# Optimization experiments

Measured on AMD Instinct MI355X. Metric: run time of the kernel, lower is better.

## Reference

```python
import jax, jax.numpy as jnp
import numpy as np

B, S, D = 2, 2048, 1024
H = 16
HD = D // H  # 64

def setup_inputs() -> dict:
    key = jax.random.key(0)
    k1, k2, k3 = jax.random.split(key, 3)
    scale = 0.02
    return {
        "x": jax.random.normal(k1, (B, S, D), dtype=jnp.float32),
        "w_qkv": jax.random.normal(k2, (D, 3 * D), dtype=jnp.float32) * scale,
        "b_qkv": jnp.zeros((3 * D,), dtype=jnp.float32),
        "w_proj": jax.random.normal(k3, (D, D), dtype=jnp.float32) * scale,
        "b_proj": jnp.zeros((D,), dtype=jnp.float32),
    }

def reference(x, w_qkv, b_qkv, w_proj, b_proj):
    batch, seq_len, _ = x.shape
    qkv = x @ w_qkv + b_qkv                      # [B,S,3D]
    qkv = qkv.reshape(batch, seq_len, 3, H, HD)
    qkv = jnp.transpose(qkv, (2, 0, 3, 1, 4))    # [3,B,H,S,HD]
    q, k, v = qkv[0], qkv[1], qkv[2]
    attn = jnp.einsum('bhqd,bhkd->bhqk', q, k) / jnp.sqrt(jnp.float32(HD))
    attn = jax.nn.softmax(attn, axis=-1)         # [B,H,S,S]
    out = jnp.einsum('bhqk,bhkd->bhqd', attn, v)
    out = jnp.transpose(out, (0, 2, 1, 3)).reshape(batch, seq_len, -1)
    return out @ w_proj + b_proj
```

## Files before the change

kernel.cpp:

```cpp
#include <hip/hip_runtime.h>
#include <math.h>

#define SS 2048
#define DD 1024
#define HH 16
#define NQKV 3072
#define MROWS 4096
#define KD 1024

typedef __attribute__((ext_vector_type(8))) short bf16x8;
typedef __attribute__((ext_vector_type(8))) unsigned short us8;
typedef __attribute__((ext_vector_type(4))) float f32x4;
typedef unsigned short u16;
typedef unsigned int u32;

#define SCALE_C 0.18033688011112042f

#define GLDS16(g, l) \
  __builtin_amdgcn_global_load_lds((const __attribute__((address_space(1))) u32*)(g), \
                                   (__attribute__((address_space(3))) u32*)(l), 16, 0, 0)

static __device__ __forceinline__ u16 f2bf(float f) {
  union { float f; u32 u; } v; v.f = f;
  u32 u = v.u;
  u += 0x7fffu + ((u >> 16) & 1u);
  return (u16)(u >> 16);
}
static __device__ __forceinline__ u32 pk2(float a, float b) {
  return (u32)f2bf(a) | ((u32)f2bf(b) << 16);
}
static __device__ __forceinline__ u32 pk2t(float a, float b) {
  union { float f; u32 u; } ua, ub; ua.f = a; ub.f = b;
  return __builtin_amdgcn_perm(ub.u, ua.u, 0x07060302u);
}

__global__ __launch_bounds__(256) void k_prep(const float* __restrict__ x,
                                              const float* __restrict__ w_qkv,
                                              const float* __restrict__ w_proj,
                                              u16* __restrict__ x_bf,
                                              u16* __restrict__ wqkvT,
                                              u16* __restrict__ wprojT) {
  __shared__ float t[64][65];
  int bx = blockIdx.x;
  int tid = threadIdx.x;
  if (bx < 2048) {
    int i = (bx * 256 + tid) * 8;
    float4 a = *(const float4*)(x + i);
    float4 b = *(const float4*)(x + i + 4);
    us8 o;
    o[0] = f2bf(a.x); o[1] = f2bf(a.y); o[2] = f2bf(a.z); o[3] = f2bf(a.w);
    o[4] = f2bf(b.x); o[5] = f2bf(b.y); o[6] = f2bf(b.z); o[7] = f2bf(b.w);
    *(us8*)(x_bf + i) = o;
    return;
  }
  const float* in; u16* out; int R = KD, C, tile;
  if (bx < 2048 + 768) { in = w_qkv; out = wqkvT; C = NQKV; tile = bx - 2048; }
  else                 { in = w_proj; out = wprojT; C = DD; tile = bx - 2816; }
  int tilesC = C >> 6;
  int tc = tile % tilesC, tr = tile / tilesC;
  int r0 = tr * 64, c0 = tc * 64;
  int lx = tid & 63, ly = tid >> 6;
#pragma unroll
  for (int i = 0; i < 16; i++) {
    int rr = ly + i * 4;
    t[rr][lx] = in[(size_t)(r0 + rr) * C + c0 + lx];
  }
  __syncthreads();
#pragma unroll
  for (int i = 0; i < 16; i++) {
    int cc = ly + i * 4;
    out[(size_t)(c0 + cc) * R + r0 + lx] = f2bf(t[lx][cc]);
  }
}

template <int MODE, int BM>
__global__ __launch_bounds__(256, 2) void k_gemm(const u16* __restrict__ A,
                                                 const u16* __restrict__ Bt,
                                                 const float* __restrict__ bias,
                                                 void* __restrict__ Cout,
                                                 u16* __restrict__ vt,
                                                 int M, int N, int K) {
  constexpr int MT = BM / 32;
  __shared__ alignas(16) u16 As[BM * 32];
  __shared__ alignas(16) u16 Bs[128 * 32];
  const int tid = threadIdx.x;
  const int w = tid >> 6, ln = tid & 63;
  const int wm = w >> 1, wn = w & 1;
  const int lm = ln & 15, quad = ln >> 4;
  const int m0 = blockIdx.y * BM, n0 = blockIdx.x * 128;
  const int lr = ln >> 2, c = ln & 3;
  const int cg = c ^ (lr & 3);

  f32x4 acc[MT][4];
#pragma unroll
  for (int i = 0; i < MT; i++)
#pragma unroll
    for (int j = 0; j < 4; j++) acc[i][j] = (f32x4){0.f, 0.f, 0.f, 0.f};

  const u16* gA0 = A  + (size_t)(m0 + 16 * w       + lr) * K + cg * 8;
  const u16* gA1 = A  + (size_t)(m0 + 16 * (w + 4) + lr) * K + cg * 8;
  const u16* gB0 = Bt + (size_t)(n0 + 16 * w       + lr) * K + cg * 8;
  const u16* gB1 = Bt + (size_t)(n0 + 16 * (w + 4) + lr) * K + cg * 8;
  char* lA0 = (char*)As + w * 1024;
  char* lA1 = (char*)As + (w + 4) * 1024;
  char* lB0 = (char*)Bs + w * 1024;
  char* lB1 = (char*)Bs + (w + 4) * 1024;

  for (int k0 = 0; k0 < K; k0 += 32) {
    GLDS16(gA0 + k0, lA0);
    if (BM == 128) GLDS16(gA1 + k0, lA1);
    GLDS16(gB0 + k0, lB0);
    GLDS16(gB1 + k0, lB1);
    __syncthreads();
    bf16x8 af[MT], bfr[4];
#pragma unroll
    for (int t = 0; t < MT; t++)
      af[t]  = *(const bf16x8*)((const char*)As + (wm * (MT * 16) + t * 16 + lm) * 64 + ((quad ^ (lm & 3)) * 16));
#pragma unroll
    for (int t = 0; t < 4; t++)
      bfr[t] = *(const bf16x8*)((const char*)Bs + (wn * 64 + t * 16 + lm) * 64 + ((quad ^ (lm & 3)) * 16));
#pragma unroll
    for (int mt = 0; mt < MT; mt++)
#pragma unroll
      for (int nt = 0; nt < 4; nt++)
        acc[mt][nt] = __builtin_amdgcn_mfma_f32_16x16x32_bf16(af[mt], bfr[nt], acc[mt][nt], 0, 0, 0);
    __syncthreads();
  }

  float bv[4];
#pragma unroll
  for (int nt = 0; nt < 4; nt++) bv[nt] = bias[n0 + wn * 64 + nt * 16 + lm];

  if (MODE == 2 && n0 >= 2 * DD) {
    int b = m0 >> 11;
    int s0 = (m0 & 2047) + wm * 64;
#pragma unroll
    for (int mt = 0; mt < MT; mt++) {
      int s = s0 + mt * 16 + quad * 4;
#pragma unroll
      for (int nt = 0; nt < 4; nt++) {
        int n = n0 + wn * 64 + nt * 16 + lm;
        int bh = b * HH + ((n - 2 * DD) >> 6);
        int d = n & 63;
        uint2 v;
        v.x = pk2(acc[mt][nt][0] + bv[nt], acc[mt][nt][1] + bv[nt]);
        v.y = pk2(acc[mt][nt][2] + bv[nt], acc[mt][nt][3] + bv[nt]);
        *(uint2*)&vt[(size_t)(bh * 64 + d) * SS + s] = v;
      }
    }
    return;
  }

  const float qs = (MODE == 2 && n0 < DD) ? SCALE_C : 1.0f;
#pragma unroll
  for (int mt = 0; mt < MT; mt++) {
#pragma unroll
    for (int r = 0; r < 4; r++) {
      int row = m0 + wm * (MT * 16) + mt * 16 + quad * 4 + r;
#pragma unroll
      for (int nt = 0; nt < 4; nt++) {
        int col = n0 + wn * 64 + nt * 16 + lm;
        float v = (acc[mt][nt][r] + bv[nt]) * qs;
        if (MODE == 2) ((u16*)Cout)[(size_t)row * N + col] = f2bf(v);
        else           ((float*)Cout)[(size_t)row * N + col] = v;
      }
    }
  }
}

__global__ __launch_bounds__(256, 3) void k_attn(const u16* __restrict__ qkv,
                                                 const u16* __restrict__ vt,
                                                 u16* __restrict__ attn) {
  __shared__ alignas(16) u16 Ks[2][64 * 64];
  __shared__ alignas(16) u16 Vs[2][64 * 64];
  __shared__ alignas(16) u16 Ps[4][16][72];

  const int tid = threadIdx.x;
  const int w = tid >> 6, ln = tid & 63;
  const int lm = ln & 15, quad = ln >> 4;
  const int bx = blockIdx.x;
  const int bh = bx >> 5;
  const int q0 = (bx & 31) * 64;
  const int b = bh >> 4, h = bh & 15;
  const size_t qkv_b = (size_t)b * SS * NQKV;
  const int hcol = h * 64;

  const int lr = ln >> 3, cc = ln & 7;
  const int cg = cc ^ lr;

  bf16x8 qf[2];
#pragma unroll
  for (int kk = 0; kk < 2; kk++)
    qf[kk] = *(const bf16x8*)(qkv + qkv_b +
               (size_t)(q0 + w * 16 + lm) * NQKV + hcol + kk * 32 + quad * 8);

  f32x4 o[4];
  float l = 0.f;
#pragma unroll
  for (int t = 0; t < 4; t++) o[t] = (f32x4){0, 0, 0, 0};

  char* psw = (char*)&Ps[w][0][0];

#pragma unroll
  for (int rr = 0; rr < 2; rr++) {
    int i = w + 4 * rr;
    GLDS16(qkv + qkv_b + (size_t)(8 * i + lr) * NQKV + DD + hcol + cg * 8, (char*)Ks[0] + i * 1024);
    GLDS16(vt + (size_t)(bh * 64 + 8 * i + lr) * SS + cg * 8,              (char*)Vs[0] + i * 1024);
  }

#pragma unroll 1
  for (int it = 0; it < SS / 64; it++) {
    __syncthreads();

    if (it + 1 < SS / 64) {
      int kv1 = (it + 1) * 64;
      char* kd = (char*)Ks[(it + 1) & 1];
      char* vd = (char*)Vs[(it + 1) & 1];
#pragma unroll
      for (int rr = 0; rr < 2; rr++) {
        int i = w + 4 * rr;
        GLDS16(qkv + qkv_b + (size_t)(kv1 + 8 * i + lr) * NQKV + DD + hcol + cg * 8, kd + i * 1024);
        GLDS16(vt + (size_t)(bh * 64 + 8 * i + lr) * SS + kv1 + cg * 8,              vd + i * 1024);
      }
    }

    const char* ksb = (const char*)Ks[it & 1];
    const char* vsb = (const char*)Vs[it & 1];

    f32x4 s[4];
#pragma unroll
    for (int t = 0; t < 4; t++) s[t] = (f32x4){0, 0, 0, 0};
#pragma unroll
    for (int kk = 0; kk < 2; kk++)
#pragma unroll
      for (int t = 0; t < 4; t++) {
        bf16x8 kf = *(const bf16x8*)(ksb + (t * 16 + lm) * 128 + (((kk * 4 + quad) ^ (lm & 7)) * 16));
        s[t] = __builtin_amdgcn_mfma_f32_16x16x32_bf16(kf, qf[kk], s[t], 0, 0, 0);
      }

    float sum = 0.f;
    u32 pkv[4][2];
#pragma unroll
    for (int t = 0; t < 4; t++) {
      float p0 = __builtin_amdgcn_exp2f(s[t][0]);
      float p1 = __builtin_amdgcn_exp2f(s[t][1]);
      float p2 = __builtin_amdgcn_exp2f(s[t][2]);
      float p3 = __builtin_amdgcn_exp2f(s[t][3]);
      sum += (p0 + p1) + (p2 + p3);
      pkv[t][0] = pk2t(p0, p1);
      pkv[t][1] = pk2t(p2, p3);
    }
    sum += __shfl_xor(sum, 16);
    sum += __shfl_xor(sum, 32);
    l += sum;
#pragma unroll
    for (int t = 0; t < 4; t++) {
      uint2 v; v.x = pkv[t][0]; v.y = pkv[t][1];
      *(uint2*)(psw + lm * 144 + t * 32 + quad * 8) = v;
    }

#pragma unroll
    for (int kk = 0; kk < 2; kk++) {
      bf16x8 pf = *(const bf16x8*)(psw + lm * 144 + kk * 64 + quad * 16);
#pragma unroll
      for (int t = 0; t < 4; t++) {
        bf16x8 vf = *(const bf16x8*)(vsb + (t * 16 + lm) * 128 + (((kk * 4 + quad) ^ (lm & 7)) * 16));
        o[t] = __builtin_amdgcn_mfma_f32_16x16x32_bf16(vf, pf, o[t], 0, 0, 0);
      }
    }
  }

  float il = 1.0f / l;
  int row = b * SS + q0 + w * 16 + lm;
#pragma unroll
  for (int t = 0; t < 4; t++) {
    uint2 v;
    v.x = pk2(o[t][0] * il, o[t][1] * il);
    v.y = pk2(o[t][2] * il, o[t][3] * il);
    *(uint2*)&attn[(size_t)row * DD + hcol + t * 16 + quad * 4] = v;
  }
}

extern "C" void kernel_launch(void* const* d_in, const int* in_sizes, int n_in,
                              void* d_out, int out_size, void* d_ws, size_t ws_size,
                              hipStream_t stream) {
  const float* x      = (const float*)d_in[0];
  const float* w_qkv  = (const float*)d_in[1];
  const float* b_qkv  = (const float*)d_in[2];
  const float* w_proj = (const float*)d_in[3];
  const float* b_proj = (const float*)d_in[4];
  float* out = (float*)d_out;

  u16* ws     = (u16*)d_ws;
  u16* x_bf   = ws;
  u16* wqkvT  = x_bf   + (size_t)MROWS * KD;
  u16* wprojT = wqkvT  + (size_t)NQKV * KD;
  u16* qkv    = wprojT + (size_t)DD * KD;
  u16* attn   = qkv    + (size_t)MROWS * NQKV;
  u16* vt     = attn   + (size_t)MROWS * DD;

  k_prep<<<3072, 256, 0, stream>>>(x, w_qkv, w_proj, x_bf, wqkvT, wprojT);
  k_gemm<2, 128><<<dim3(NQKV / 128, MROWS / 128), 256, 0, stream>>>(x_bf, wqkvT, b_qkv, qkv, vt, MROWS, NQKV, KD);
  k_attn<<<2 * HH * (SS / 64), 256, 0, stream>>>(qkv, vt, attn);
  k_gemm<0, 64><<<dim3(DD / 128, MROWS / 64), 256, 0, stream>>>(attn, wprojT, b_proj, out, nullptr, MROWS, DD, KD);
}
```

Before: 209.2 us.

## Split attention KV range in two halves with combine kernel, 128-row query tiles

The attention kernel now has each block process 128 query rows (two 16-row sub-tiles per wave) against half of the key/value sequence, so K/V tiles loaded into LDS are reused across twice as many queries. Partial unnormalized outputs and row sums are written to reused workspace buffers (x_bf and wqkvT), and a new combine kernel sums the halves and normalizes. It also swizzles the P scratch layout and raises the occupancy hint. The cost is an extra kernel launch, extra bf16 partial-output traffic, and double rounding of the partials to bf16.

Result: no change. 210.0 us (+0.4%).

```diff
diff --git a/kernel.cpp b/kernel.cpp
--- a/kernel.cpp
+++ b/kernel.cpp
@@ -25,6 +25,9 @@
   u32 u = v.u;
   u += 0x7fffu + ((u >> 16) & 1u);
   return (u16)(u >> 16);
+}
+static __device__ __forceinline__ float bf2f(u16 x) {
+  union { u32 u; float f; } v; v.u = ((u32)x) << 16; return v.f;
 }
 static __device__ __forceinline__ u32 pk2(float a, float b) {
   return (u32)f2bf(a) | ((u32)f2bf(b) << 16);
@@ -168,52 +171,63 @@
   }
 }
 
-__global__ __launch_bounds__(256, 3) void k_attn(const u16* __restrict__ qkv,
+__global__ __launch_bounds__(256, 4) void k_attn(const u16* __restrict__ qkv,
                                                  const u16* __restrict__ vt,
-                                                 u16* __restrict__ attn) {
+                                                 u16* __restrict__ po0,
+                                                 u16* __restrict__ po1,
+                                                 float* __restrict__ lb0,
+                                                 float* __restrict__ lb1) {
   __shared__ alignas(16) u16 Ks[2][64 * 64];
   __shared__ alignas(16) u16 Vs[2][64 * 64];
-  __shared__ alignas(16) u16 Ps[4][16][72];
+  __shared__ alignas(16) u16 Ps[4 * 16 * 64];
 
   const int tid = threadIdx.x;
   const int w = tid >> 6, ln = tid & 63;
   const int lm = ln & 15, quad = ln >> 4;
   const int bx = blockIdx.x;
-  const int bh = bx >> 5;
-  const int q0 = (bx & 31) * 64;
+  const int half = bx >> 9;
+  const int bxx = bx & 511;
+  const int bh = bxx >> 4;
+  const int q0 = (bxx & 15) * 128;
   const int b = bh >> 4, h = bh & 15;
   const size_t qkv_b = (size_t)b * SS * NQKV;
   const int hcol = h * 64;
+  const int kvoff = half * (SS / 2);
+
+  u16* __restrict__ po = half ? po1 : po0;
+  float* __restrict__ lb = half ? lb1 : lb0;
 
   const int lr = ln >> 3, cc = ln & 7;
   const int cg = cc ^ lr;
 
-  bf16x8 qf[2];
-#pragma unroll
-  for (int kk = 0; kk < 2; kk++)
-    qf[kk] = *(const bf16x8*)(qkv + qkv_b +
-               (size_t)(q0 + w * 16 + lm) * NQKV + hcol + kk * 32 + quad * 8);
-
-  f32x4 o[4];
-  float l = 0.f;
-#pragma unroll
-  for (int t = 0; t < 4; t++) o[t] = (f32x4){0, 0, 0, 0};
-
-  char* psw = (char*)&Ps[w][0][0];
+  bf16x8 qf[2][2];
+#pragma unroll
+  for (int qs2 = 0; qs2 < 2; qs2++)
+#pragma unroll
+    for (int kk = 0; kk < 2; kk++)
+      qf[qs2][kk] = *(const bf16x8*)(qkv + qkv_b +
+                     (size_t)(q0 + w * 32 + qs2 * 16 + lm) * NQKV + hcol + kk * 32 + quad * 8);
+
+  f32x4 o[4][2];
+  float l[2] = {0.f, 0.f};
+#pragma unroll
+  for (int t = 0; t < 4; t++) { o[t][0] = (f32x4){0, 0, 0, 0}; o[t][1] = (f32x4){0, 0, 0, 0}; }
+
+  char* psw = (char*)Ps + w * 2048;
 
 #pragma unroll
   for (int rr = 0; rr < 2; rr++) {
     int i = w + 4 * rr;
-    GLDS16(qkv + qkv_b + (size_t)(8 * i + lr) * NQKV + DD + hcol + cg * 8, (char*)Ks[0] + i * 1024);
-    GLDS16(vt + (size_t)(bh * 64 + 8 * i + lr) * SS + cg * 8,              (char*)Vs[0] + i * 1024);
+    GLDS16(qkv + qkv_b + (size_t)(kvoff + 8 * i + lr) * NQKV + DD + hcol + cg * 8, (char*)Ks[0] + i * 1024);
+    GLDS16(vt + (size_t)(bh * 64 + 8 * i + lr) * SS + kvoff + cg * 8,              (char*)Vs[0] + i * 1024);
   }
 
 #pragma unroll 1
-  for (int it = 0; it < SS / 64; it++) {
+  for (int it = 0; it < 16; it++) {
     __syncthreads();
 
-    if (it + 1 < SS / 64) {
-      int kv1 = (it + 1) * 64;
+    if (it + 1 < 16) {
+      int kv1 = kvoff + (it + 1) * 64;
       char* kd = (char*)Ks[(it + 1) & 1];
       char* vd = (char*)Vs[(it + 1) & 1];
 #pragma unroll
@@ -227,58 +241,87 @@
     const char* ksb = (const char*)Ks[it & 1];
     const char* vsb = (const char*)Vs[it & 1];
 
-    f32x4 s[4];
-#pragma unroll
-    for (int t = 0; t < 4; t++) s[t] = (f32x4){0, 0, 0, 0};
+    f32x4 s[4][2];
+#pragma unroll
+    for (int t = 0; t < 4; t++) { s[t][0] = (f32x4){0, 0, 0, 0}; s[t][1] = (f32x4){0, 0, 0, 0}; }
 #pragma unroll
     for (int kk = 0; kk < 2; kk++)
 #pragma unroll
       for (int t = 0; t < 4; t++) {
         bf16x8 kf = *(const bf16x8*)(ksb + (t * 16 + lm) * 128 + (((kk * 4 + quad) ^ (lm & 7)) * 16));
-        s[t] = __builtin_amdgcn_mfma_f32_16x16x32_bf16(kf, qf[kk], s[t], 0, 0, 0);
-      }
-
-    float sum = 0.f;
-    u32 pkv[4][2];
+        s[t][0] = __builtin_amdgcn_mfma_f32_16x16x32_bf16(kf, qf[0][kk], s[t][0], 0, 0, 0);
+        s[t][1] = __builtin_amdgcn_mfma_f32_16x16x32_bf16(kf, qf[1][kk], s[t][1], 0, 0, 0);
+      }
+
+    bf16x8 vf[2][4];
+#pragma unroll
+    for (int kk = 0; kk < 2; kk++)
+#pragma unroll
+      for (int t = 0; t < 4; t++)
+        vf[kk][t] = *(const bf16x8*)(vsb + (t * 16 + lm) * 128 + (((kk * 4 + quad) ^ (lm & 7)) * 16));
+
+#pragma unroll
+    for (int qs2 = 0; qs2 < 2; qs2++) {
+      float sum = 0.f;
+      u32 pkv[4][2];
+#pragma unroll
+      for (int t = 0; t < 4; t++) {
+        float p0 = __builtin_amdgcn_exp2f(s[t][qs2][0]);
+        float p1 = __builtin_amdgcn_exp2f(s[t][qs2][1]);
+        float p2 = __builtin_amdgcn_exp2f(s[t][qs2][2]);
+        float p3 = __builtin_amdgcn_exp2f(s[t][qs2][3]);
+        sum += (p0 + p1) + (p2 + p3);
+        pkv[t][0] = pk2t(p0, p1);
+        pkv[t][1] = pk2t(p2, p3);
+      }
+      sum += __shfl_xor(sum, 16);
+      sum += __shfl_xor(sum, 32);
+      l[qs2] += sum;
+#pragma unroll
+      for (int t = 0; t < 4; t++) {
+        uint2 v; v.x = pkv[t][0]; v.y = pkv[t][1];
+        *(uint2*)(psw + lm * 128 + (((2 * t + (quad >> 1)) ^ (lm & 7)) * 16) + (quad & 1) * 8) = v;
+      }
+      bf16x8 pf0 = *(const bf16x8*)(psw + lm * 128 + (((0 + quad) ^ (lm & 7)) * 16));
+      bf16x8 pf1 = *(const bf16x8*)(psw + lm * 128 + (((4 + quad) ^ (lm & 7)) * 16));
+#pragma unroll
+      for (int t = 0; t < 4; t++) {
+        o[t][qs2] = __builtin_amdgcn_mfma_f32_16x16x32_bf16(vf[0][t], pf0, o[t][qs2], 0, 0, 0);
+        o[t][qs2] = __builtin_amdgcn_mfma_f32_16x16x32_bf16(vf[1][t], pf1, o[t][qs2], 0, 0, 0);
+      }
+    }
+  }
+
+#pragma unroll
+  for (int qs2 = 0; qs2 < 2; qs2++) {
+    int qg = q0 + w * 32 + qs2 * 16 + lm;
+    if (quad == 0) lb[(size_t)bh * SS + qg] = l[qs2];
+    int row = b * SS + qg;
 #pragma unroll
     for (int t = 0; t < 4; t++) {
-      float p0 = __builtin_amdgcn_exp2f(s[t][0]);
-      float p1 = __builtin_amdgcn_exp2f(s[t][1]);
-      float p2 = __builtin_amdgcn_exp2f(s[t][2]);
-      float p3 = __builtin_amdgcn_exp2f(s[t][3]);
-      sum += (p0 + p1) + (p2 + p3);
-      pkv[t][0] = pk2t(p0, p1);
-      pkv[t][1] = pk2t(p2, p3);
-    }
-    sum += __shfl_xor(sum, 16);
-    sum += __shfl_xor(sum, 32);
-    l += sum;
-#pragma unroll
-    for (int t = 0; t < 4; t++) {
-      uint2 v; v.x = pkv[t][0]; v.y = pkv[t][1];
-      *(uint2*)(psw + lm * 144 + t * 32 + quad * 8) = v;
-    }
-
-#pragma unroll
-    for (int kk = 0; kk < 2; kk++) {
-      bf16x8 pf = *(const bf16x8*)(psw + lm * 144 + kk * 64 + quad * 16);
-#pragma unroll
-      for (int t = 0; t < 4; t++) {
-        bf16x8 vf = *(const bf16x8*)(vsb + (t * 16 + lm) * 128 + (((kk * 4 + quad) ^ (lm & 7)) * 16));
-        o[t] = __builtin_amdgcn_mfma_f32_16x16x32_bf16(vf, pf, o[t], 0, 0, 0);
-      }
-    }
-  }
-
-  float il = 1.0f / l;
-  int row = b * SS + q0 + w * 16 + lm;
-#pragma unroll
-  for (int t = 0; t < 4; t++) {
-    uint2 v;
-    v.x = pk2(o[t][0] * il, o[t][1] * il);
-    v.y = pk2(o[t][2] * il, o[t][3] * il);
-    *(uint2*)&attn[(size_t)row * DD + hcol + t * 16 + quad * 4] = v;
-  }
+      uint2 v;
+      v.x = pk2(o[t][qs2][0], o[t][qs2][1]);
+      v.y = pk2(o[t][qs2][2], o[t][qs2][3]);
+      *(uint2*)&po[(size_t)row * DD + hcol + t * 16 + quad * 4] = v;
+    }
+  }
+}
+
+__global__ __launch_bounds__(256) void k_comb(u16* __restrict__ po0,
+                                              const u16* __restrict__ po1,
+                                              const float* __restrict__ l0,
+                                              const float* __restrict__ l1) {
+  int i = (blockIdx.x * 256 + threadIdx.x) * 8;
+  int row = i >> 10, col = i & 1023;
+  int h = col >> 6, b = row >> 11, q = row & 2047;
+  size_t li = (size_t)(b * HH + h) * SS + q;
+  float il = 1.0f / (l0[li] + l1[li]);
+  us8 a = *(const us8*)(po0 + i);
+  us8 p = *(const us8*)(po1 + i);
+  us8 o;
+#pragma unroll
+  for (int j = 0; j < 8; j++) o[j] = f2bf((bf2f(a[j]) + bf2f(p[j])) * il);
+  *(us8*)(po0 + i) = o;
 }
 
 extern "C" void kernel_launch(void* const* d_in, const int* in_sizes, int n_in,
@@ -299,8 +342,12 @@
   u16* attn   = qkv    + (size_t)MROWS * NQKV;
   u16* vt     = attn   + (size_t)MROWS * DD;
 
+  float* l0 = (float*)wqkvT;
+  float* l1 = l0 + (size_t)2 * HH * SS;
+
   k_prep<<<3072, 256, 0, stream>>>(x, w_qkv, w_proj, x_bf, wqkvT, wprojT);
   k_gemm<2, 128><<<dim3(NQKV / 128, MROWS / 128), 256, 0, stream>>>(x_bf, wqkvT, b_qkv, qkv, vt, MROWS, NQKV, KD);
-  k_attn<<<2 * HH * (SS / 64), 256, 0, stream>>>(qkv, vt, attn);
+  k_attn<<<2 * 2 * HH * (SS / 128), 256, 0, stream>>>(qkv, vt, attn, x_bf, l0, l1);
+  k_comb<<<(MROWS * DD) / (256 * 8), 256, 0, stream>>>(attn, x_bf, l0, l1);
   k_gemm<0, 64><<<dim3(DD / 128, MROWS / 64), 256, 0, stream>>>(attn, wprojT, b_proj, out, nullptr, MROWS, DD, KD);
 }
```
